# Kernel optimization log

Measured on AMD Instinct MI355X. Metric: run time of the kernel, lower is better.

The kernel has to match this reference:

```python
import math
import jax, jax.numpy as jnp
import numpy as np

E = 8          # num_experts
H = 1024       # hidden_dim
F = 2048       # ffn_dim
TOP_K = 2
CAP_FACTOR = 1.25
B, S = 2, 2048


def setup_inputs() -> dict:
    key = jax.random.key(0)
    ks = jax.random.split(key, 7)
    xavier_gu = math.sqrt(2.0 / (H + F))
    return {
        "x": jax.random.normal(ks[0], (B, S, H), dtype=jnp.float32),
        "router_weight": 0.01 * jax.random.normal(ks[1], (H, E), dtype=jnp.float32),
        "w_gate": xavier_gu * jax.random.normal(ks[2], (E, H, F), dtype=jnp.float32),
        "w_up": xavier_gu * jax.random.normal(ks[3], (E, H, F), dtype=jnp.float32),
        "w_down": xavier_gu * jax.random.normal(ks[4], (E, F, H), dtype=jnp.float32),
        "ln_gamma": jnp.ones((H,), dtype=jnp.float32),
        "ln_beta": jnp.zeros((H,), dtype=jnp.float32),
    }


def _layernorm(x, g, b, eps=1e-5):
    mu = x.mean(-1, keepdims=True)
    var = ((x - mu) ** 2).mean(-1, keepdims=True)
    return (x - mu) / jnp.sqrt(var + eps) * g + b


def reference(x, router_weight, w_gate, w_up, w_down, ln_gamma, ln_beta):
    Bd, Sd, Hd = x.shape
    T = Bd * Sd
    cap = int(math.ceil(CAP_FACTOR * T / E))  # static capacity per expert

    residual = x
    tokens = _layernorm(x, ln_gamma, ln_beta).reshape(T, Hd)

    # ---- router: softmax + top-k + renormalize ----
    logits = tokens @ router_weight                      # (T, E) fp32
    probs = jax.nn.softmax(logits, axis=-1)
    wts, idx = jax.lax.top_k(probs, TOP_K)               # (T, K)
    wts = wts / wts.sum(-1, keepdims=True)

    # ---- dispatch: first-come-first-served up to capacity per expert ----
    mask_all = (idx[None, :, :] == jnp.arange(E)[:, None, None]).any(-1)  # (E, T)
    # stable argsort puts routed token indices (in order) first
    sel = jnp.argsort(jnp.where(mask_all, 0, 1), axis=1, stable=True)[:, :cap]  # (E, cap)
    valid = jnp.take_along_axis(mask_all, sel, axis=1)   # (E, cap)
    xin = tokens[sel] * valid[..., None]                 # (E, cap, H); zeros for empty slots

    # ---- grouped SwiGLU expert GEMMs ----
    gate = jax.nn.silu(jnp.einsum('ech,ehf->ecf', xin, w_gate))
    up = jnp.einsum('ech,ehf->ecf', xin, w_up)
    expert_outputs = jnp.einsum('ecf,efh->ech', gate * up, w_down)  # (E, cap, H)

    # ---- scatter-gather combine (slot = min(t, cap-1), per reference impl) ----
    slot = jnp.minimum(jnp.arange(T), cap - 1)           # (T,)
    gathered = expert_outputs[idx, slot[:, None]]        # (T, K, H)
    out = (wts[..., None] * gathered).sum(axis=1)        # (T, H)

    return out.reshape(Bd, Sd, Hd) + residual
```

## Files before the change

### kernel.cpp

```cpp
#include <hip/hip_runtime.h>
#include <hip/hip_bf16.h>

#define NE 8
#define NH 1024
#define NF 2048
#define NT_TOK 4096
#define CAP 640
#define CAPP 768

typedef __bf16 bf16x8 __attribute__((ext_vector_type(8)));
typedef float f32x4 __attribute__((ext_vector_type(4)));

__device__ __forceinline__ ushort f2bf(float f) {
    union { float f; unsigned u; } v; v.f = f;
    unsigned r = (v.u + 0x7FFFu + ((v.u >> 16) & 1u)) >> 16;
    return (ushort)r;
}

__device__ __forceinline__ void glds16(const ushort* g, ushort* l) {
    __builtin_amdgcn_global_load_lds((const __attribute__((address_space(1))) void*)g,
                                     (__attribute__((address_space(3))) void*)l,
                                     16, 0, 0);
}

#define MFMA_BF16 __builtin_amdgcn_mfma_f32_16x16x32_bf16

__global__ __launch_bounds__(256) void k_conv_t(
    const float* __restrict__ in, ushort* __restrict__ out, int R, int C)
{
    int e = blockIdx.z;
    int c  = blockIdx.x * 64 + (threadIdx.x & 63);
    int rb = blockIdx.y * 128 + (threadIdx.x >> 6) * 32;
    in  += (size_t)e * R * C;
    out += (size_t)e * R * C;
    float v[32];
    #pragma unroll
    for (int j = 0; j < 32; ++j) v[j] = in[(size_t)(rb + j) * C + c];
    #pragma unroll
    for (int q = 0; q < 4; ++q) {
        union { ushort sh[8]; uint4 u; } p;
        #pragma unroll
        for (int j = 0; j < 8; ++j) p.sh[j] = f2bf(v[q * 8 + j]);
        *(uint4*)(out + (size_t)c * R + rb + q * 8) = p.u;
    }
}

__global__ __launch_bounds__(256) void k_ln_router(
    const float* __restrict__ x, const float* __restrict__ rw,
    const float* __restrict__ gamma, const float* __restrict__ beta,
    ushort* __restrict__ tok_bf, int* __restrict__ idx, float* __restrict__ wts)
{
    int t = blockIdx.x, tid = threadIdx.x;
    int lane = tid & 63, wid = tid >> 6;
    const float* xp = x + (size_t)t * NH;

    float4 v = *(const float4*)(xp + tid * 4);
    float xs[4] = {v.x, v.y, v.z, v.w};
    float s = xs[0] + xs[1] + xs[2] + xs[3];
    float q = xs[0]*xs[0] + xs[1]*xs[1] + xs[2]*xs[2] + xs[3]*xs[3];

    __shared__ float rs[4], rq[4], rl[4][8];
    #pragma unroll
    for (int o = 32; o; o >>= 1) { s += __shfl_xor(s, o); q += __shfl_xor(q, o); }
    if (lane == 0) { rs[wid] = s; rq[wid] = q; }
    __syncthreads();
    float S = rs[0] + rs[1] + rs[2] + rs[3];
    float Q = rq[0] + rq[1] + rq[2] + rq[3];
    float mean = S * (1.0f / NH);
    float var  = Q * (1.0f / NH) - mean * mean;
    float rstd = 1.0f / sqrtf(var + 1e-5f);

    float le[8] = {0,0,0,0,0,0,0,0};
    ushort tb[4];
    #pragma unroll
    for (int j = 0; j < 4; ++j) {
        int h = tid * 4 + j;
        float nh = (xs[j] - mean) * rstd * gamma[h] + beta[h];
        tb[j] = f2bf(nh);
        float4 r0 = *(const float4*)(rw + h * 8);
        float4 r1 = *(const float4*)(rw + h * 8 + 4);
        le[0] += nh * r0.x; le[1] += nh * r0.y; le[2] += nh * r0.z; le[3] += nh * r0.w;
        le[4] += nh * r1.x; le[5] += nh * r1.y; le[6] += nh * r1.z; le[7] += nh * r1.w;
    }
    union { ushort s2[4]; uint2 u2; } pk;
    pk.s2[0]=tb[0]; pk.s2[1]=tb[1]; pk.s2[2]=tb[2]; pk.s2[3]=tb[3];
    *(uint2*)(tok_bf + (size_t)t * NH + tid * 4) = pk.u2;

    #pragma unroll
    for (int o = 32; o; o >>= 1)
        #pragma unroll
        for (int e = 0; e < 8; ++e) le[e] += __shfl_xor(le[e], o);
    if (lane == 0)
        #pragma unroll
        for (int e = 0; e < 8; ++e) rl[wid][e] = le[e];
    __syncthreads();

    if (tid == 0) {
        float l[8];
        #pragma unroll
        for (int e = 0; e < 8; ++e) l[e] = rl[0][e] + rl[1][e] + rl[2][e] + rl[3][e];
        float mx = l[0];
        #pragma unroll
        for (int e = 1; e < 8; ++e) mx = fmaxf(mx, l[e]);
        float p[8], den = 0.f;
        #pragma unroll
        for (int e = 0; e < 8; ++e) { p[e] = expf(l[e] - mx); den += p[e]; }
        float rden = 1.0f / den;
        #pragma unroll
        for (int e = 0; e < 8; ++e) p[e] *= rden;
        int i0 = 0; float b0 = p[0];
        #pragma unroll
        for (int e = 1; e < 8; ++e) if (p[e] > b0) { b0 = p[e]; i0 = e; }
        int i1 = (i0 == 0) ? 1 : 0; float b1 = p[i1];
        #pragma unroll
        for (int e = 0; e < 8; ++e) if (e != i0 && p[e] > b1) { b1 = p[e]; i1 = e; }
        float sw = 1.0f / (b0 + b1);
        idx[2*t] = i0; idx[2*t+1] = i1;
        wts[2*t] = b0 * sw; wts[2*t+1] = b1 * sw;
    }
}

__global__ __launch_bounds__(1024) void k_build_sel(
    const int* __restrict__ idx, int* __restrict__ sel)
{
    int e = blockIdx.x, tid = threadIdx.x;
    int lane = tid & 63, wid = tid >> 6;
    __shared__ int wsum[16], wpre[16], sbase;
    if (tid < CAPP) sel[e * CAPP + tid] = -1;
    if (tid == 0) sbase = 0;
    __syncthreads();

    for (int ch = 0; ch < NT_TOK / 1024; ++ch) {
        int t = ch * 1024 + tid;
        int m = (idx[2*t] == e || idx[2*t+1] == e) ? 1 : 0;
        int v = m;
        #pragma unroll
        for (int d = 1; d < 64; d <<= 1) {
            int u = __shfl_up(v, d);
            if (lane >= d) v += u;
        }
        if (lane == 63) wsum[wid] = v;
        __syncthreads();
        if (tid < 16) {
            int ws = wsum[tid], wv = ws;
            #pragma unroll
            for (int d = 1; d < 16; d <<= 1) {
                int u = __shfl_up(wv, d);
                if (tid >= d) wv += u;
            }
            wpre[tid] = wv - ws;
        }
        __syncthreads();
        int base0 = sbase;
        int slot = base0 + wpre[wid] + v - m;
        if (m && slot < CAP) sel[e * CAPP + slot] = t;
        __syncthreads();
        if (tid == 0) sbase = base0 + wpre[15] + wsum[15];
        __syncthreads();
    }
}

__global__ __launch_bounds__(256) void k_gather(
    const int* __restrict__ sel, const ushort* __restrict__ tok,
    ushort* __restrict__ xin)
{
    int sIdx = blockIdx.x;
    int tokid = sel[sIdx];
    uint2 v = make_uint2(0u, 0u);
    if (tokid >= 0)
        v = *(const uint2*)(tok + (size_t)tokid * NH + threadIdx.x * 4);
    *(uint2*)(xin + (size_t)sIdx * NH + threadIdx.x * 4) = v;
}


__global__ __launch_bounds__(512, 2) void k_gemm1(
    const ushort* __restrict__ xin, const ushort* __restrict__ wgT,
    const ushort* __restrict__ wuT, ushort* __restrict__ hb)
{
    __shared__ __align__(16) ushort As[4][8192];
    __shared__ __align__(16) ushort Bgs[4][4096];
    __shared__ __align__(16) ushort Bus[4][4096];

    int e = blockIdx.z, mb = blockIdx.y, nb = blockIdx.x;
    const ushort* A  = xin + (size_t)e * CAPP * NH + (size_t)mb * 256 * NH;
    const ushort* Bg = wgT + (size_t)e * NF * NH + (size_t)nb * 128 * NH;
    const ushort* Bu = wuT + (size_t)e * NF * NH + (size_t)nb * 128 * NH;

    int tid = threadIdx.x, lane = tid & 63, wid = tid >> 6;
    int wm = wid >> 2, wn = wid & 3;
    int lr = lane & 15, lq = lane >> 4;

    int Rg = tid >> 3;
    int ug = (tid & 7) ^ (Rg & 7);
    int sROW2 = ug >> 2;
    int sCOL  = (ug & 3) * 8;
    size_t aoffg0 = (size_t)(2 * Rg + sROW2) * NH + sCOL;
    size_t aoffg1 = (size_t)(2 * (64 + Rg) + sROW2) * NH + sCOL;
    size_t boffg  = (size_t)(2 * Rg + sROW2) * NH + sCOL;
    int aldsu0 = (wid * 8) * 64;
    int aldsu1 = (64 + wid * 8) * 64;
    int bldsu  = wid * 512;

    int aoff[8], goff[2];
    #pragma unroll
    for (int m = 0; m < 8; ++m) {
        int a = wm * 128 + m * 16 + lr;
        int Rr = a >> 1;
        int sl = (((a & 1) << 2) | lq) ^ (Rr & 7);
        aoff[m] = Rr * 64 + sl * 8;
    }
    #pragma unroll
    for (int n = 0; n < 2; ++n) {
        int nn = wn * 32 + n * 16 + lr;
        int Rr = nn >> 1;
        int sl = (((nn & 1) << 2) | lq) ^ (Rr & 7);
        goff[n] = Rr * 64 + sl * 8;
    }

    f32x4 accg[8][2] = {}; f32x4 accu[8][2] = {};

    const int NT = NH / 32;

    #define STAGE1(t) do { int _sl = (t) & 3; int _k0 = (t) * 32;               \
        glds16(A  + aoffg0 + _k0, &As[_sl][aldsu0]);                            \
        glds16(A  + aoffg1 + _k0, &As[_sl][aldsu1]);                            \
        glds16(Bg + boffg  + _k0, &Bgs[_sl][bldsu]);                            \
        glds16(Bu + boffg  + _k0, &Bus[_sl][bldsu]); } while (0)

    STAGE1(0); STAGE1(1);
    asm volatile("s_waitcnt vmcnt(4)" ::: "memory");
    asm volatile("s_barrier" ::: "memory");

    for (int t = 0; t < NT; ++t) {
        int slot = t & 3;
        bool pf = (t + 2 < NT);
        if (pf) STAGE1(t + 2);
        const ushort* Ab = &As[slot][0];
        const ushort* Gb = &Bgs[slot][0];
        const ushort* Ub = &Bus[slot][0];
        bf16x8 af[8], bg[2], bu[2];
        #pragma unroll
        for (int m = 0; m < 8; ++m) af[m] = *(const bf16x8*)&Ab[aoff[m]];
        #pragma unroll
        for (int n = 0; n < 2; ++n) {
            bg[n] = *(const bf16x8*)&Gb[goff[n]];
            bu[n] = *(const bf16x8*)&Ub[goff[n]];
        }
        __builtin_amdgcn_s_setprio(1);
        #pragma unroll
        for (int m = 0; m < 8; ++m)
            #pragma unroll
            for (int n = 0; n < 2; ++n) {
                accg[m][n] = MFMA_BF16(af[m], bg[n], accg[m][n], 0, 0, 0);
                accu[m][n] = MFMA_BF16(af[m], bu[n], accu[m][n], 0, 0, 0);
            }
        __builtin_amdgcn_s_setprio(0);
        if (pf) asm volatile("s_waitcnt vmcnt(4)" ::: "memory");
        else    asm volatile("s_waitcnt vmcnt(0)" ::: "memory");
        asm volatile("s_barrier" ::: "memory");
    }
    #undef STAGE1

    ushort* outp = hb + (size_t)e * CAPP * NF + (size_t)mb * 256 * NF + nb * 128;
    #pragma unroll
    for (int m = 0; m < 8; ++m)
        #pragma unroll
        for (int n = 0; n < 2; ++n)
            #pragma unroll
            for (int r = 0; r < 4; ++r) {
                int row = wm * 128 + m * 16 + lq * 4 + r;
                int col = wn * 32 + n * 16 + lr;
                float g = accg[m][n][r], u = accu[m][n][r];
                float sg = g / (1.0f + expf(-g));
                outp[(size_t)row * NF + col] = f2bf(sg * u);
            }
}

__global__ __launch_bounds__(512, 2) void k_gemm2(
    const ushort* __restrict__ hb, const ushort* __restrict__ wdT,
    float* __restrict__ eo)
{
    __shared__ __align__(16) ushort As[4][8192];
    __shared__ __align__(16) ushort Bs[4][4096];

    int e = blockIdx.z, mb = blockIdx.y, nb = blockIdx.x;
    const ushort* A = hb  + (size_t)e * CAPP * NF + (size_t)mb * 256 * NF;
    const ushort* B = wdT + (size_t)e * NH * NF + (size_t)nb * 128 * NF;

    int tid = threadIdx.x, lane = tid & 63, wid = tid >> 6;
    int wm = wid >> 1, wn = wid & 1;
    int lr = lane & 15, lq = lane >> 4;

    int Rg = tid >> 3;
    int ug = (tid & 7) ^ (Rg & 7);
    int sROW2 = ug >> 2;
    int sCOL  = (ug & 3) * 8;
    size_t aoffg0 = (size_t)(2 * Rg + sROW2) * NF + sCOL;
    size_t aoffg1 = (size_t)(2 * (64 + Rg) + sROW2) * NF + sCOL;
    size_t boffg  = (size_t)(2 * Rg + sROW2) * NF + sCOL;
    int aldsu0 = (wid * 8) * 64;
    int aldsu1 = (64 + wid * 8) * 64;
    int bldsu  = wid * 512;

    int aoff[4], boff[4];
    #pragma unroll
    for (int m = 0; m < 4; ++m) {
        int a = wm * 64 + m * 16 + lr;
        int Rr = a >> 1;
        int sl = (((a & 1) << 2) | lq) ^ (Rr & 7);
        aoff[m] = Rr * 64 + sl * 8;
    }
    #pragma unroll
    for (int n = 0; n < 4; ++n) {
        int nn = wn * 64 + n * 16 + lr;
        int Rr = nn >> 1;
        int sl = (((nn & 1) << 2) | lq) ^ (Rr & 7);
        boff[n] = Rr * 64 + sl * 8;
    }

    f32x4 acc[4][4] = {};

    const int NT = NF / 32;

    #define STAGE2(t) do { int _sl = (t) & 3; int _k0 = (t) * 32;               \
        glds16(A + aoffg0 + _k0, &As[_sl][aldsu0]);                             \
        glds16(A + aoffg1 + _k0, &As[_sl][aldsu1]);                             \
        glds16(B + boffg  + _k0, &Bs[_sl][bldsu]); } while (0)

    STAGE2(0); STAGE2(1);
    asm volatile("s_waitcnt vmcnt(3)" ::: "memory");
    asm volatile("s_barrier" ::: "memory");

    for (int t = 0; t < NT; ++t) {
        int slot = t & 3;
        bool pf = (t + 2 < NT);
        if (pf) STAGE2(t + 2);
        const ushort* Ab = &As[slot][0];
        const ushort* Bb = &Bs[slot][0];
        bf16x8 af[4], bf_[4];
        #pragma unroll
        for (int m = 0; m < 4; ++m) af[m] = *(const bf16x8*)&Ab[aoff[m]];
        #pragma unroll
        for (int n = 0; n < 4; ++n) bf_[n] = *(const bf16x8*)&Bb[boff[n]];
        __builtin_amdgcn_s_setprio(1);
        #pragma unroll
        for (int m = 0; m < 4; ++m)
            #pragma unroll
            for (int n = 0; n < 4; ++n)
                acc[m][n] = MFMA_BF16(af[m], bf_[n], acc[m][n], 0, 0, 0);
        __builtin_amdgcn_s_setprio(0);
        if (pf) asm volatile("s_waitcnt vmcnt(3)" ::: "memory");
        else    asm volatile("s_waitcnt vmcnt(0)" ::: "memory");
        asm volatile("s_barrier" ::: "memory");
    }
    #undef STAGE2

    float* outp = eo + (size_t)e * CAPP * NH + (size_t)mb * 256 * NH + nb * 128;
    #pragma unroll
    for (int m = 0; m < 4; ++m)
        #pragma unroll
        for (int n = 0; n < 4; ++n)
            #pragma unroll
            for (int r = 0; r < 4; ++r) {
                int row = wm * 64 + m * 16 + lq * 4 + r;
                int col = wn * 64 + n * 16 + lr;
                outp[(size_t)row * NH + col] = acc[m][n][r];
            }
}

__global__ __launch_bounds__(256) void k_final(
    const float* __restrict__ x, const float* __restrict__ eo,
    const int* __restrict__ idx, const float* __restrict__ wts,
    float* __restrict__ out)
{
    int t = blockIdx.x;
    int c = (t < CAP - 1) ? t : (CAP - 1);
    int e0 = idx[2*t], e1 = idx[2*t+1];
    float w0 = wts[2*t], w1 = wts[2*t+1];
    int h = threadIdx.x * 4;
    float4 xv = *(const float4*)(x + (size_t)t * NH + h);
    float4 a = *(const float4*)(eo + ((size_t)e0 * CAPP + c) * NH + h);
    float4 b = *(const float4*)(eo + ((size_t)e1 * CAPP + c) * NH + h);
    float4 o;
    o.x = xv.x + w0 * a.x + w1 * b.x;
    o.y = xv.y + w0 * a.y + w1 * b.y;
    o.z = xv.z + w0 * a.z + w1 * b.z;
    o.w = xv.w + w0 * a.w + w1 * b.w;
    *(float4*)(out + (size_t)t * NH + h) = o;
}

extern "C" void kernel_launch(void* const* d_in, const int* in_sizes, int n_in,
                              void* d_out, int out_size, void* d_ws, size_t ws_size,
                              hipStream_t stream)
{
    const float* x     = (const float*)d_in[0];
    const float* rw    = (const float*)d_in[1];
    const float* wg    = (const float*)d_in[2];
    const float* wu    = (const float*)d_in[3];
    const float* wd    = (const float*)d_in[4];
    const float* gamma = (const float*)d_in[5];
    const float* beta  = (const float*)d_in[6];
    float* out = (float*)d_out;

    char* ws = (char*)d_ws;
    float*  eo     = (float*) (ws);
    ushort* tok_bf = (ushort*)(ws);
    ushort* xin    = (ushort*)(ws +  25165824);
    ushort* hb     = (ushort*)(ws +  37748736);
    ushort* wgT    = (ushort*)(ws +  62914560);
    ushort* wuT    = (ushort*)(ws +  96468992);
    ushort* wdT    = (ushort*)(ws + 130023424);
    int*    idx    = (int*)   (ws + 163577856);
    float*  wts    = (float*) (ws + 163610624);
    int*    sel    = (int*)   (ws + 163643392);

    k_conv_t<<<dim3(NF / 64, NH / 128, NE), 256, 0, stream>>>(wg, wgT, NH, NF);
    k_conv_t<<<dim3(NF / 64, NH / 128, NE), 256, 0, stream>>>(wu, wuT, NH, NF);
    k_conv_t<<<dim3(NH / 64, NF / 128, NE), 256, 0, stream>>>(wd, wdT, NF, NH);

    k_ln_router<<<NT_TOK, 256, 0, stream>>>(x, rw, gamma, beta, tok_bf, idx, wts);
    k_build_sel<<<NE, 1024, 0, stream>>>(idx, sel);
    k_gather<<<NE * CAPP, 256, 0, stream>>>(sel, tok_bf, xin);
    k_gemm1<<<dim3(NF / 128, CAPP / 256, NE), 512, 0, stream>>>(xin, wgT, wuT, hb);
    k_gemm2<<<dim3(NH / 128, CAPP / 256, NE), 512, 0, stream>>>(hb, wdT, eo);
    k_final<<<NT_TOK, 256, 0, stream>>>(x, eo, idx, wts, out);
}
```

Baseline: 443.1 us.

## Drop capacity padding, shrink GEMM tiles to 128 rows, and fuse weight transposes via LDS

Removes the padding of per-expert capacity from 768 to 640 rows, so the GEMMs no longer compute on the 128 padded rows. GEMM tiles shrink to 128 rows with a 3-stage LDS ring, and gemm2 drops to 256 threads, aiming for more resident blocks per CU. The three weight-transpose launches become one kernel that stages through LDS with coalesced float4 reads and vector writes. Smaller tiles lower operand reuse per block and raise weight traffic per output, which is the trade-off.

Result: faster. 383.5 us (-13.5%).

```diff
diff --git a/kernel.cpp b/kernel.cpp
--- a/kernel.cpp
+++ b/kernel.cpp
@@ -6,7 +6,6 @@
 #define NF 2048
 #define NT_TOK 4096
 #define CAP 640
-#define CAPP 768
 
 typedef __bf16 bf16x8 __attribute__((ext_vector_type(8)));
 typedef float f32x4 __attribute__((ext_vector_type(4)));
@@ -25,23 +24,42 @@
 
 #define MFMA_BF16 __builtin_amdgcn_mfma_f32_16x16x32_bf16
 
+#define LR 132
+
 __global__ __launch_bounds__(256) void k_conv_t(
-    const float* __restrict__ in, ushort* __restrict__ out, int R, int C)
-{
-    int e = blockIdx.z;
-    int c  = blockIdx.x * 64 + (threadIdx.x & 63);
-    int rb = blockIdx.y * 128 + (threadIdx.x >> 6) * 32;
-    in  += (size_t)e * R * C;
-    out += (size_t)e * R * C;
-    float v[32];
-    #pragma unroll
-    for (int j = 0; j < 32; ++j) v[j] = in[(size_t)(rb + j) * C + c];
-    #pragma unroll
-    for (int q = 0; q < 4; ++q) {
-        union { ushort sh[8]; uint4 u; } p;
-        #pragma unroll
-        for (int j = 0; j < 8; ++j) p.sh[j] = f2bf(v[q * 8 + j]);
-        *(uint4*)(out + (size_t)c * R + rb + q * 8) = p.u;
+    const float* __restrict__ wg, const float* __restrict__ wu,
+    const float* __restrict__ wd, ushort* __restrict__ wgT,
+    ushort* __restrict__ wuT, ushort* __restrict__ wdT)
+{
+    int z = blockIdx.z;
+    const float* in; ushort* out; int R, C;
+    if (z < 8)       { in = wg + (size_t)z * NH * NF;        out = wgT + (size_t)z * NH * NF;        R = NH; C = NF; }
+    else if (z < 16) { in = wu + (size_t)(z - 8) * NH * NF;  out = wuT + (size_t)(z - 8) * NH * NF;  R = NH; C = NF; }
+    else             { in = wd + (size_t)(z - 16) * NF * NH; out = wdT + (size_t)(z - 16) * NF * NH; R = NF; C = NH; }
+    int c0 = blockIdx.x * 64, r0 = blockIdx.y * 128;
+    if (c0 >= C || r0 >= R) return;
+
+    __shared__ __align__(16) ushort lds[64 * LR];
+    int tid = threadIdx.x;
+    int rr = tid >> 4;
+    int cc = (tid & 15) * 4;
+    #pragma unroll
+    for (int it = 0; it < 8; ++it) {
+        int r = it * 16 + rr;
+        float4 v = *(const float4*)(in + (size_t)(r0 + r) * C + c0 + cc);
+        lds[(cc + 0) * LR + r] = f2bf(v.x);
+        lds[(cc + 1) * LR + r] = f2bf(v.y);
+        lds[(cc + 2) * LR + r] = f2bf(v.z);
+        lds[(cc + 3) * LR + r] = f2bf(v.w);
+    }
+    __syncthreads();
+    int cb = tid >> 5;
+    int r4 = (tid & 31) * 4;
+    #pragma unroll
+    for (int it = 0; it < 8; ++it) {
+        int cI = it * 8 + cb;
+        uint2 v = *(const uint2*)&lds[cI * LR + r4];
+        *(uint2*)(out + (size_t)(c0 + cI) * R + r0 + r4) = v;
     }
 }
 
@@ -126,7 +144,7 @@
     int e = blockIdx.x, tid = threadIdx.x;
     int lane = tid & 63, wid = tid >> 6;
     __shared__ int wsum[16], wpre[16], sbase;
-    if (tid < CAPP) sel[e * CAPP + tid] = -1;
+    if (tid < CAP) sel[e * CAP + tid] = -1;
     if (tid == 0) sbase = 0;
     __syncthreads();
 
@@ -153,7 +171,7 @@
         __syncthreads();
         int base0 = sbase;
         int slot = base0 + wpre[wid] + v - m;
-        if (m && slot < CAP) sel[e * CAPP + slot] = t;
+        if (m && slot < CAP) sel[e * CAP + slot] = t;
         __syncthreads();
         if (tid == 0) sbase = base0 + wpre[15] + wsum[15];
         __syncthreads();
@@ -173,16 +191,16 @@
 }
 
 
-__global__ __launch_bounds__(512, 2) void k_gemm1(
+__global__ __launch_bounds__(512, 4) void k_gemm1(
     const ushort* __restrict__ xin, const ushort* __restrict__ wgT,
     const ushort* __restrict__ wuT, ushort* __restrict__ hb)
 {
-    __shared__ __align__(16) ushort As[4][8192];
-    __shared__ __align__(16) ushort Bgs[4][4096];
-    __shared__ __align__(16) ushort Bus[4][4096];
+    __shared__ __align__(16) ushort As[3][4096];
+    __shared__ __align__(16) ushort Bgs[3][4096];
+    __shared__ __align__(16) ushort Bus[3][4096];
 
     int e = blockIdx.z, mb = blockIdx.y, nb = blockIdx.x;
-    const ushort* A  = xin + (size_t)e * CAPP * NH + (size_t)mb * 256 * NH;
+    const ushort* A  = xin + (size_t)e * CAP * NH + (size_t)mb * 128 * NH;
     const ushort* Bg = wgT + (size_t)e * NF * NH + (size_t)nb * 128 * NH;
     const ushort* Bu = wuT + (size_t)e * NF * NH + (size_t)nb * 128 * NH;
 
@@ -192,83 +210,77 @@
 
     int Rg = tid >> 3;
     int ug = (tid & 7) ^ (Rg & 7);
-    int sROW2 = ug >> 2;
-    int sCOL  = (ug & 3) * 8;
-    size_t aoffg0 = (size_t)(2 * Rg + sROW2) * NH + sCOL;
-    size_t aoffg1 = (size_t)(2 * (64 + Rg) + sROW2) * NH + sCOL;
-    size_t boffg  = (size_t)(2 * Rg + sROW2) * NH + sCOL;
-    int aldsu0 = (wid * 8) * 64;
-    int aldsu1 = (64 + wid * 8) * 64;
-    int bldsu  = wid * 512;
-
-    int aoff[8], goff[2];
-    #pragma unroll
-    for (int m = 0; m < 8; ++m) {
-        int a = wm * 128 + m * 16 + lr;
+    size_t goff = (size_t)(2 * Rg + (ug >> 2)) * NH + (ug & 3) * 8;
+    int ldsu = tid * 8;
+
+    int aoff[4], boff[2];
+    #pragma unroll
+    for (int m = 0; m < 4; ++m) {
+        int a = wm * 64 + m * 16 + lr;
         int Rr = a >> 1;
         int sl = (((a & 1) << 2) | lq) ^ (Rr & 7);
         aoff[m] = Rr * 64 + sl * 8;
     }
     #pragma unroll
     for (int n = 0; n < 2; ++n) {
-        int nn = wn * 32 + n * 16 + lr;
-        int Rr = nn >> 1;
-        int sl = (((nn & 1) << 2) | lq) ^ (Rr & 7);
-        goff[n] = Rr * 64 + sl * 8;
-    }
-
-    f32x4 accg[8][2] = {}; f32x4 accu[8][2] = {};
-
+        int c = wn * 32 + n * 16 + lr;
+        int Rr = c >> 1;
+        int sl = (((c & 1) << 2) | lq) ^ (Rr & 7);
+        boff[n] = Rr * 64 + sl * 8;
+    }
+
+    f32x4 accg[4][2] = {}; f32x4 accu[4][2] = {};
     const int NT = NH / 32;
 
-    #define STAGE1(t) do { int _sl = (t) & 3; int _k0 = (t) * 32;               \
-        glds16(A  + aoffg0 + _k0, &As[_sl][aldsu0]);                            \
-        glds16(A  + aoffg1 + _k0, &As[_sl][aldsu1]);                            \
-        glds16(Bg + boffg  + _k0, &Bgs[_sl][bldsu]);                            \
-        glds16(Bu + boffg  + _k0, &Bus[_sl][bldsu]); } while (0)
-
-    STAGE1(0); STAGE1(1);
-    asm volatile("s_waitcnt vmcnt(4)" ::: "memory");
+    #define STG1(t, s) do { size_t _k = (size_t)(t) * 32;                       \
+        glds16(A  + goff + _k, &As[s][ldsu]);                                   \
+        glds16(Bg + goff + _k, &Bgs[s][ldsu]);                                  \
+        glds16(Bu + goff + _k, &Bus[s][ldsu]); } while (0)
+
+    STG1(0, 0); STG1(1, 1);
+    asm volatile("s_waitcnt vmcnt(3)" ::: "memory");
     asm volatile("s_barrier" ::: "memory");
 
+    int sl_c = 0, sl_p = 2;
     for (int t = 0; t < NT; ++t) {
-        int slot = t & 3;
         bool pf = (t + 2 < NT);
-        if (pf) STAGE1(t + 2);
-        const ushort* Ab = &As[slot][0];
-        const ushort* Gb = &Bgs[slot][0];
-        const ushort* Ub = &Bus[slot][0];
-        bf16x8 af[8], bg[2], bu[2];
-        #pragma unroll
-        for (int m = 0; m < 8; ++m) af[m] = *(const bf16x8*)&Ab[aoff[m]];
+        if (pf) STG1(t + 2, sl_p);
+        const ushort* Ab = &As[sl_c][0];
+        const ushort* Gb = &Bgs[sl_c][0];
+        const ushort* Ub = &Bus[sl_c][0];
+        bf16x8 af[4], bg[2], bu[2];
+        #pragma unroll
+        for (int m = 0; m < 4; ++m) af[m] = *(const bf16x8*)&Ab[aoff[m]];
         #pragma unroll
         for (int n = 0; n < 2; ++n) {
-            bg[n] = *(const bf16x8*)&Gb[goff[n]];
-            bu[n] = *(const bf16x8*)&Ub[goff[n]];
+            bg[n] = *(const bf16x8*)&Gb[boff[n]];
+            bu[n] = *(const bf16x8*)&Ub[boff[n]];
         }
         __builtin_amdgcn_s_setprio(1);
         #pragma unroll
-        for (int m = 0; m < 8; ++m)
+        for (int m = 0; m < 4; ++m)
             #pragma unroll
             for (int n = 0; n < 2; ++n) {
                 accg[m][n] = MFMA_BF16(af[m], bg[n], accg[m][n], 0, 0, 0);
                 accu[m][n] = MFMA_BF16(af[m], bu[n], accu[m][n], 0, 0, 0);
             }
         __builtin_amdgcn_s_setprio(0);
-        if (pf) asm volatile("s_waitcnt vmcnt(4)" ::: "memory");
+        if (pf) asm volatile("s_waitcnt vmcnt(3)" ::: "memory");
         else    asm volatile("s_waitcnt vmcnt(0)" ::: "memory");
         asm volatile("s_barrier" ::: "memory");
-    }
-    #undef STAGE1
-
-    ushort* outp = hb + (size_t)e * CAPP * NF + (size_t)mb * 256 * NF + nb * 128;
-    #pragma unroll
-    for (int m = 0; m < 8; ++m)
+        sl_c = (sl_c == 2) ? 0 : sl_c + 1;
+        sl_p = (sl_p == 2) ? 0 : sl_p + 1;
+    }
+    #undef STG1
+
+    ushort* outp = hb + (size_t)e * CAP * NF + (size_t)mb * 128 * NF + nb * 128;
+    #pragma unroll
+    for (int m = 0; m < 4; ++m)
         #pragma unroll
         for (int n = 0; n < 2; ++n)
             #pragma unroll
             for (int r = 0; r < 4; ++r) {
-                int row = wm * 128 + m * 16 + lq * 4 + r;
+                int row = wm * 64 + m * 16 + lq * 4 + r;
                 int col = wn * 32 + n * 16 + lr;
                 float g = accg[m][n][r], u = accu[m][n][r];
                 float sg = g / (1.0f + expf(-g));
@@ -276,15 +288,15 @@
             }
 }
 
-__global__ __launch_bounds__(512, 2) void k_gemm2(
+__global__ __launch_bounds__(256, 4) void k_gemm2(
     const ushort* __restrict__ hb, const ushort* __restrict__ wdT,
     float* __restrict__ eo)
 {
-    __shared__ __align__(16) ushort As[4][8192];
-    __shared__ __align__(16) ushort Bs[4][4096];
+    __shared__ __align__(16) ushort As[3][4096];
+    __shared__ __align__(16) ushort Bs[3][4096];
 
     int e = blockIdx.z, mb = blockIdx.y, nb = blockIdx.x;
-    const ushort* A = hb  + (size_t)e * CAPP * NF + (size_t)mb * 256 * NF;
+    const ushort* A = hb  + (size_t)e * CAP * NF + (size_t)mb * 128 * NF;
     const ushort* B = wdT + (size_t)e * NH * NF + (size_t)nb * 128 * NF;
 
     int tid = threadIdx.x, lane = tid & 63, wid = tid >> 6;
@@ -293,14 +305,10 @@
 
     int Rg = tid >> 3;
     int ug = (tid & 7) ^ (Rg & 7);
-    int sROW2 = ug >> 2;
-    int sCOL  = (ug & 3) * 8;
-    size_t aoffg0 = (size_t)(2 * Rg + sROW2) * NF + sCOL;
-    size_t aoffg1 = (size_t)(2 * (64 + Rg) + sROW2) * NF + sCOL;
-    size_t boffg  = (size_t)(2 * Rg + sROW2) * NF + sCOL;
-    int aldsu0 = (wid * 8) * 64;
-    int aldsu1 = (64 + wid * 8) * 64;
-    int bldsu  = wid * 512;
+    int sROW2 = ug >> 2, sCOL = (ug & 3) * 8;
+    size_t goff0 = (size_t)(2 * Rg + sROW2) * NF + sCOL;
+    size_t goff1 = (size_t)(2 * (32 + Rg) + sROW2) * NF + sCOL;
+    int ldsu = tid * 8;
 
     int aoff[4], boff[4];
     #pragma unroll
@@ -312,31 +320,31 @@
     }
     #pragma unroll
     for (int n = 0; n < 4; ++n) {
-        int nn = wn * 64 + n * 16 + lr;
-        int Rr = nn >> 1;
-        int sl = (((nn & 1) << 2) | lq) ^ (Rr & 7);
+        int c = wn * 64 + n * 16 + lr;
+        int Rr = c >> 1;
+        int sl = (((c & 1) << 2) | lq) ^ (Rr & 7);
         boff[n] = Rr * 64 + sl * 8;
     }
 
     f32x4 acc[4][4] = {};
-
     const int NT = NF / 32;
 
-    #define STAGE2(t) do { int _sl = (t) & 3; int _k0 = (t) * 32;               \
-        glds16(A + aoffg0 + _k0, &As[_sl][aldsu0]);                             \
-        glds16(A + aoffg1 + _k0, &As[_sl][aldsu1]);                             \
-        glds16(B + boffg  + _k0, &Bs[_sl][bldsu]); } while (0)
-
-    STAGE2(0); STAGE2(1);
-    asm volatile("s_waitcnt vmcnt(3)" ::: "memory");
+    #define STG2(t, s) do { size_t _k = (size_t)(t) * 32;                       \
+        glds16(A + goff0 + _k, &As[s][ldsu]);                                   \
+        glds16(A + goff1 + _k, &As[s][2048 + ldsu]);                            \
+        glds16(B + goff0 + _k, &Bs[s][ldsu]);                                   \
+        glds16(B + goff1 + _k, &Bs[s][2048 + ldsu]); } while (0)
+
+    STG2(0, 0); STG2(1, 1);
+    asm volatile("s_waitcnt vmcnt(4)" ::: "memory");
     asm volatile("s_barrier" ::: "memory");
 
+    int sl_c = 0, sl_p = 2;
     for (int t = 0; t < NT; ++t) {
-        int slot = t & 3;
         bool pf = (t + 2 < NT);
-        if (pf) STAGE2(t + 2);
-        const ushort* Ab = &As[slot][0];
-        const ushort* Bb = &Bs[slot][0];
+        if (pf) STG2(t + 2, sl_p);
+        const ushort* Ab = &As[sl_c][0];
+        const ushort* Bb = &Bs[sl_c][0];
         bf16x8 af[4], bf_[4];
         #pragma unroll
         for (int m = 0; m < 4; ++m) af[m] = *(const bf16x8*)&Ab[aoff[m]];
@@ -349,13 +357,15 @@
             for (int n = 0; n < 4; ++n)
                 acc[m][n] = MFMA_BF16(af[m], bf_[n], acc[m][n], 0, 0, 0);
         __builtin_amdgcn_s_setprio(0);
-        if (pf) asm volatile("s_waitcnt vmcnt(3)" ::: "memory");
+        if (pf) asm volatile("s_waitcnt vmcnt(4)" ::: "memory");
         else    asm volatile("s_waitcnt vmcnt(0)" ::: "memory");
         asm volatile("s_barrier" ::: "memory");
-    }
-    #undef STAGE2
-
-    float* outp = eo + (size_t)e * CAPP * NH + (size_t)mb * 256 * NH + nb * 128;
+        sl_c = (sl_c == 2) ? 0 : sl_c + 1;
+        sl_p = (sl_p == 2) ? 0 : sl_p + 1;
+    }
+    #undef STG2
+
+    float* outp = eo + (size_t)e * CAP * NH + (size_t)mb * 128 * NH + nb * 128;
     #pragma unroll
     for (int m = 0; m < 4; ++m)
         #pragma unroll
@@ -379,8 +389,8 @@
     float w0 = wts[2*t], w1 = wts[2*t+1];
     int h = threadIdx.x * 4;
     float4 xv = *(const float4*)(x + (size_t)t * NH + h);
-    float4 a = *(const float4*)(eo + ((size_t)e0 * CAPP + c) * NH + h);
-    float4 b = *(const float4*)(eo + ((size_t)e1 * CAPP + c) * NH + h);
+    float4 a = *(const float4*)(eo + ((size_t)e0 * CAP + c) * NH + h);
+    float4 b = *(const float4*)(eo + ((size_t)e1 * CAP + c) * NH + h);
     float4 o;
     o.x = xv.x + w0 * a.x + w1 * b.x;
     o.y = xv.y + w0 * a.y + w1 * b.y;
@@ -405,23 +415,21 @@
     char* ws = (char*)d_ws;
     float*  eo     = (float*) (ws);
     ushort* tok_bf = (ushort*)(ws);
-    ushort* xin    = (ushort*)(ws +  25165824);
-    ushort* hb     = (ushort*)(ws +  37748736);
-    ushort* wgT    = (ushort*)(ws +  62914560);
-    ushort* wuT    = (ushort*)(ws +  96468992);
-    ushort* wdT    = (ushort*)(ws + 130023424);
-    int*    idx    = (int*)   (ws + 163577856);
-    float*  wts    = (float*) (ws + 163610624);
-    int*    sel    = (int*)   (ws + 163643392);
-
-    k_conv_t<<<dim3(NF / 64, NH / 128, NE), 256, 0, stream>>>(wg, wgT, NH, NF);
-    k_conv_t<<<dim3(NF / 64, NH / 128, NE), 256, 0, stream>>>(wu, wuT, NH, NF);
-    k_conv_t<<<dim3(NH / 64, NF / 128, NE), 256, 0, stream>>>(wd, wdT, NF, NH);
+    ushort* xin    = (ushort*)(ws +  20971520);
+    ushort* hb     = (ushort*)(ws +  31457280);
+    ushort* wgT    = (ushort*)(ws +  52428800);
+    ushort* wuT    = (ushort*)(ws +  85983232);
+    ushort* wdT    = (ushort*)(ws + 119537664);
+    int*    idx    = (int*)   (ws + 153092096);
+    float*  wts    = (float*) (ws + 153124864);
+    int*    sel    = (int*)   (ws + 153157632);
+
+    k_conv_t<<<dim3(32, 16, 24), 256, 0, stream>>>(wg, wu, wd, wgT, wuT, wdT);
 
     k_ln_router<<<NT_TOK, 256, 0, stream>>>(x, rw, gamma, beta, tok_bf, idx, wts);
     k_build_sel<<<NE, 1024, 0, stream>>>(idx, sel);
-    k_gather<<<NE * CAPP, 256, 0, stream>>>(sel, tok_bf, xin);
-    k_gemm1<<<dim3(NF / 128, CAPP / 256, NE), 512, 0, stream>>>(xin, wgT, wuT, hb);
-    k_gemm2<<<dim3(NH / 128, CAPP / 256, NE), 512, 0, stream>>>(hb, wdT, eo);
+    k_gather<<<NE * CAP, 256, 0, stream>>>(sel, tok_bf, xin);
+    k_gemm1<<<dim3(NF / 128, CAP / 128, NE), 512, 0, stream>>>(xin, wgT, wuT, hb);
+    k_gemm2<<<dim3(NH / 128, CAP / 128, NE), 256, 0, stream>>>(hb, wdT, eo);
     k_final<<<NT_TOK, 256, 0, stream>>>(x, eo, idx, wts, out);
 }
```
